# Kernel optimization log

Hardware: AMD Instinct MI355X
Metric: run time of the kernel (lower is better)

## Reference

```python
import jax, jax.numpy as jnp
import numpy as np

N_NODES = 50000
N_EDGES = 500000
NUM_RADIAL = 6
HIDDEN = 128

def swish(v):
    return v * jax.nn.sigmoid(v)

def setup_inputs() -> dict:
    key = jax.random.key(0)
    ks = jax.random.split(key, 8)
    x = jax.random.randint(ks[0], (N_NODES,), 0, 95, dtype=jnp.int32)
    rbf = jax.random.normal(ks[1], (N_EDGES, NUM_RADIAL), dtype=jnp.float32)
    i = jax.random.randint(ks[2], (N_EDGES,), 0, N_NODES, dtype=jnp.int32)
    j = jax.random.randint(ks[3], (N_EDGES,), 0, N_NODES, dtype=jnp.int32)
    sqrt3 = np.sqrt(3.0).astype(np.float32)
    emb_weight = jax.random.uniform(ks[4], (95, HIDDEN), minval=-sqrt3, maxval=sqrt3, dtype=jnp.float32)
    w_rbf0 = jax.random.normal(ks[5], (HIDDEN, NUM_RADIAL), dtype=jnp.float32) * 0.2
    b_rbf0 = jnp.zeros((HIDDEN,), dtype=jnp.float32)
    w_lin = jax.random.normal(ks[6], (HIDDEN, 3 * HIDDEN), dtype=jnpp.float32) if False else jax.random.normal(ks[6], (HIDDEN, 3 * HIDDEN), dtype=jnp.float32) * 0.05
    b_lin = jnp.zeros((HIDDEN,), dtype=jnp.float32)
    w_rbf1 = jax.random.normal(ks[7], (HIDDEN, NUM_RADIAL), dtype=jnp.float32) * 0.4
    return {"x": x, "rbf": rbf, "i": i, "j": j, "emb_weight": emb_weight,
            "w_rbf0": w_rbf0, "b_rbf0": b_rbf0, "w_lin": w_lin, "b_lin": b_lin,
            "w_rbf1": w_rbf1}

def reference(x, rbf, i, j, emb_weight, w_rbf0, b_rbf0, w_lin, b_lin, w_rbf1):
    # node embedding lookup: [N, H]
    h = emb_weight[x]
    # rbf0 = swish(rbf @ W0^T + b0): [E, H]
    rbf0 = swish(jnp.einsum('er,hr->eh', rbf, w_rbf0) + b_rbf0)
    # gather endpoint embeddings and concat with rbf0: [E, 3H]
    cat = jnp.concatenate([h[i], h[j], rbf0], axis=-1)
    e1 = swish(jnp.einsum('ek,hk->eh', cat, w_lin) + b_lin)
    e2 = jnp.einsum('er,hr->eh', rbf, w_rbf1) * e1
    return (e1, e2)
```

## Files before the change

### kernel.cpp

```cpp
#include <hip/hip_runtime.h>

#define HIDDEN 128
#define NRAD 6
#define NEMB 95

typedef short bf16x8 __attribute__((ext_vector_type(8)));
typedef float f32x4 __attribute__((ext_vector_type(4)));

__device__ __forceinline__ float fast_rcp(float x) { return __builtin_amdgcn_rcpf(x); }
__device__ __forceinline__ float swishf(float v) { return v * fast_rcp(1.0f + __expf(-v)); }
__device__ __forceinline__ short f2bf(float f) {
    union { float f; unsigned u; } c; c.f = f;
    unsigned r = (c.u + 0x7FFFu + ((c.u >> 16) & 1u)) >> 16;
    return (short)(unsigned short)r;
}
__device__ __forceinline__ float bf2f(unsigned short u) {
    union { unsigned u; float f; } c; c.u = ((unsigned)u) << 16; return c.f;
}
__device__ __forceinline__ unsigned pk(float lo, float hi) {
    return __builtin_amdgcn_perm(__float_as_uint(hi), __float_as_uint(lo), 0x07060302u);
}
__device__ __forceinline__ float xlo(unsigned u) {
    union { unsigned u; float f; } c; c.u = u << 16; return c.f;
}
__device__ __forceinline__ float xhi(unsigned u) {
    union { unsigned u; float f; } c; c.u = u & 0xffff0000u; return c.f;
}
__device__ __forceinline__ void barrier_lgkm() {
    asm volatile("s_waitcnt lgkmcnt(0)" ::: "memory");
    __builtin_amdgcn_s_barrier();
}
__device__ __forceinline__ void wait_lgkm() {
    asm volatile("s_waitcnt lgkmcnt(0)" ::: "memory");
}

__global__ void precompute_kernel(const float* __restrict__ emb,
                                  const float* __restrict__ w_lin,
                                  const float* __restrict__ b_lin,
                                  unsigned* __restrict__ pPair) {
    __shared__ __align__(16) float erow[HIDDEN];
    const int a = blockIdx.x;
    const int h = threadIdx.x;
    erow[h] = emb[a * HIDDEN + h];
    __syncthreads();
    float a1 = b_lin[h];
    float a2 = 0.f;
    const float* __restrict__ w1 = w_lin + h * 384;
    const float* __restrict__ w2 = w1 + HIDDEN;
#pragma unroll 8
    for (int k = 0; k < HIDDEN; ++k) {
        a1 += erow[k] * w1[k];
        a2 += erow[k] * w2[k];
    }
    const unsigned lo = (unsigned)(unsigned short)f2bf(a1);
    const unsigned hi = ((unsigned)(unsigned short)f2bf(a2)) << 16;
    pPair[a * HIDDEN + h] = hi | lo;
}

struct RawMD {
    float2 ra, rb, rc;
    int ii, jj;
};

__device__ __forceinline__ RawMD load_raw(int st, int l15, int n_edges,
                                          const int* __restrict__ iv,
                                          const int* __restrict__ jv,
                                          const float* __restrict__ rbf) {
    int e = st * 16 + l15;
    int ecl = (e < n_edges) ? e : (n_edges - 1);
    RawMD m;
    const float2* rp = reinterpret_cast<const float2*>(rbf + (size_t)ecl * NRAD);
    m.ra = rp[0];
    m.rb = rp[1];
    m.rc = rp[2];
    m.ii = iv[ecl];
    m.jj = jv[ecl];
    return m;
}

__global__ __launch_bounds__(256, 2)
void edge_mfma_kernel(const int* __restrict__ xv,
                      const float* __restrict__ rbf,
                      const int* __restrict__ iv,
                      const int* __restrict__ jv,
                      const float* __restrict__ w_rbf0,
                      const float* __restrict__ b_rbf0,
                      const float* __restrict__ w_rbf1,
                      const float* __restrict__ w_lin,
                      const unsigned* __restrict__ pPairG,
                      float* __restrict__ out_e1,
                      float* __restrict__ out_e2,
                      int n_edges, int tiles_per_block, int nt32, int n_rows) {
    __shared__ unsigned pps[NEMB * HIDDEN];
    __shared__ __align__(16) short fragS[2][16 * 132];
    __shared__ __align__(8) unsigned short stg[4][2][32 * 36];
    __shared__ __align__(16) short w1a[HIDDEN * 8];

    const int tid = threadIdx.x;

    {
        const int n = (n_rows < NEMB ? n_rows : NEMB) * HIDDEN;
        for (int s = tid; s < n; s += 256) pps[s] = pPairG[s];
    }
    if (tid < HIDDEN) {
        bf16x8 f1;
#pragma unroll
        for (int r = 0; r < NRAD; ++r) f1[r] = f2bf(w_rbf1[tid * NRAD + r]);
        f1[6] = 0; f1[7] = 0;
        *reinterpret_cast<bf16x8*>(&w1a[tid * 8]) = f1;
    }

    const int wid = tid >> 6;
    const int lane = tid & 63;
    const int l15 = lane & 15;
    const int lg = lane >> 4;

    const int kbase = wid * 32 + lg * 8;
    float w0r[8][6], b0r[8];
#pragma unroll
    for (int j = 0; j < 8; ++j) {
        const float2* wp = reinterpret_cast<const float2*>(w_rbf0 + (kbase + j) * NRAD);
        const float2 a = wp[0], b = wp[1], c = wp[2];
        w0r[j][0] = a.x; w0r[j][1] = a.y;
        w0r[j][2] = b.x; w0r[j][3] = b.y;
        w0r[j][4] = c.x; w0r[j][5] = c.y;
        b0r[j] = b_rbf0[kbase + j];
    }

    bf16x8 w3f[2][4];
#pragma unroll
    for (int n2 = 0; n2 < 2; ++n2) {
        const int h = (wid * 2 + n2) * 16 + l15;
        const float* wp = w_lin + h * 384 + 256;
#pragma unroll
        for (int ks = 0; ks < 4; ++ks) {
            const float4* s4 = reinterpret_cast<const float4*>(wp + (ks * 4 + lg) * 8);
            const float4 va = s4[0];
            const float4 vb = s4[1];
            bf16x8 fr;
            fr[0] = f2bf(va.x); fr[1] = f2bf(va.y);
            fr[2] = f2bf(va.z); fr[3] = f2bf(va.w);
            fr[4] = f2bf(vb.x); fr[5] = f2bf(vb.y);
            fr[6] = f2bf(vb.z); fr[7] = f2bf(vb.w);
            w3f[n2][ks] = fr;
        }
    }
    __syncthreads();

    const int bt = blockIdx.x * tiles_per_block;
    const int btEnd = min(bt + tiles_per_block, nt32);
    if (bt >= btEnd) return;

    const f32x4 zero4 = (f32x4){0.f, 0.f, 0.f, 0.f};

    RawMD c0 = load_raw(2 * bt,     l15, n_edges, iv, jv, rbf);
    RawMD c1 = load_raw(2 * bt + 1, l15, n_edges, iv, jv, rbf);
    RawMD x0 = load_raw(2 * bt + 2, l15, n_edges, iv, jv, rbf);
    RawMD x1 = load_raw(2 * bt + 3, l15, n_edges, iv, jv, rbf);
    int c0i = xv[c0.ii], c0j = xv[c0.jj];
    int c1i = xv[c1.ii], c1j = xv[c1.jj];

    for (int t = bt; t < btEnd; ++t) {
        RawMD p0 = load_raw(2 * (t + 2),     l15, n_edges, iv, jv, rbf);
        RawMD p1 = load_raw(2 * (t + 2) + 1, l15, n_edges, iv, jv, rbf);
        const int g0i = xv[x0.ii], g0j = xv[x0.jj];
        const int g1i = xv[x1.ii], g1j = xv[x1.jj];

        {
            float sv[8];
#pragma unroll
            for (int j = 0; j < 8; ++j) {
                float tv = b0r[j]
                         + c0.ra.x * w0r[j][0] + c0.ra.y * w0r[j][1]
                         + c0.rb.x * w0r[j][2] + c0.rb.y * w0r[j][3]
                         + c0.rc.x * w0r[j][4] + c0.rc.y * w0r[j][5];
                sv[j] = swishf(tv);
            }
            uint4 mf;
            mf.x = pk(sv[0], sv[1]); mf.y = pk(sv[2], sv[3]);
            mf.z = pk(sv[4], sv[5]); mf.w = pk(sv[6], sv[7]);
            *reinterpret_cast<uint4*>(&fragS[0][(wid * 4 + lg) * 132 + l15 * 8]) = mf;
        }
        {
            float sv[8];
#pragma unroll
            for (int j = 0; j < 8; ++j) {
                float tv = b0r[j]
                         + c1.ra.x * w0r[j][0] + c1.ra.y * w0r[j][1]
                         + c1.rb.x * w0r[j][2] + c1.rb.y * w0r[j][3]
                         + c1.rc.x * w0r[j][4] + c1.rc.y * w0r[j][5];
                sv[j] = swishf(tv);
            }
            uint4 mf;
            mf.x = pk(sv[0], sv[1]); mf.y = pk(sv[2], sv[3]);
            mf.z = pk(sv[4], sv[5]); mf.w = pk(sv[6], sv[7]);
            *reinterpret_cast<uint4*>(&fragS[1][(wid * 4 + lg) * 132 + l15 * 8]) = mf;
        }

        union { uint4 u; bf16x8 b; } rp0, rp1;
        rp0.u = (uint4){0u, 0u, 0u, 0u};
        rp1.u = (uint4){0u, 0u, 0u, 0u};
        if (lg == 0) {
            rp0.u.x = pk(c0.ra.x, c0.ra.y);
            rp0.u.y = pk(c0.rb.x, c0.rb.y);
            rp0.u.z = pk(c0.rc.x, c0.rc.y);
            rp1.u.x = pk(c1.ra.x, c1.ra.y);
            rp1.u.y = pk(c1.rb.x, c1.rb.y);
            rp1.u.z = pk(c1.rc.x, c1.rc.y);
        }
        f32x4 acc2[2][2];
#pragma unroll
        for (int n2 = 0; n2 < 2; ++n2) {
            const bf16x8 aw = *reinterpret_cast<const bf16x8*>(
                &w1a[((wid * 2 + n2) * 16 + l15) * 8]);
            acc2[0][n2] = __builtin_amdgcn_mfma_f32_16x16x32_bf16(aw, rp0.b, zero4, 0, 0, 0);
            acc2[1][n2] = __builtin_amdgcn_mfma_f32_16x16x32_bf16(aw, rp1.b, zero4, 0, 0, 0);
        }

        barrier_lgkm();

        f32x4 acc[2][2];
#pragma unroll
        for (int u = 0; u < 2; ++u) {
            bf16x8 bf[4];
#pragma unroll
            for (int ks = 0; ks < 4; ++ks)
                bf[ks] = *reinterpret_cast<const bf16x8*>(
                    &fragS[u][(ks * 4 + lg) * 132 + l15 * 8]);
#pragma unroll
            for (int n2 = 0; n2 < 2; ++n2) acc[u][n2] = zero4;
#pragma unroll
            for (int ks = 0; ks < 4; ++ks)
#pragma unroll
                for (int n2 = 0; n2 < 2; ++n2)
                    acc[u][n2] = __builtin_amdgcn_mfma_f32_16x16x32_bf16(
                        w3f[n2][ks], bf[ks], acc[u][n2], 0, 0, 0);
        }

        barrier_lgkm();

        if (t != bt) {
            const int tp = t - 1;
#pragma unroll
            for (int arr = 0; arr < 2; ++arr) {
                float* __restrict__ ob = arr ? out_e2 : out_e1;
#pragma unroll
                for (int s = 0; s < 4; ++s) {
                    const int e = 8 * s + (lane >> 3);
                    const uint2 u2v = *reinterpret_cast<const uint2*>(
                        &stg[wid][arr][e * 36 + (lane & 7) * 4]);
                    const int eg = tp * 32 + e;
                    if (eg < n_edges) {
                        f32x4 v;
                        v[0] = xlo(u2v.x); v[1] = xhi(u2v.x);
                        v[2] = xlo(u2v.y); v[3] = xhi(u2v.y);
                        *reinterpret_cast<f32x4*>(
                            ob + (size_t)eg * HIDDEN + wid * 32 + (lane & 7) * 4) = v;
                    }
                }
            }
        }
        wait_lgkm();

#pragma unroll
        for (int u = 0; u < 2; ++u) {
            const int xi = u ? c1i : c0i;
            const int xj = u ? c1j : c0j;
            const int row = u * 16 + l15;
#pragma unroll
            for (int n2 = 0; n2 < 2; ++n2) {
                const int ch0 = wid * 32 + n2 * 16 + lg * 4;
                const uint4 r1 = *reinterpret_cast<const uint4*>(&pps[xi * HIDDEN + ch0]);
                const uint4 r2 = *reinterpret_cast<const uint4*>(&pps[xj * HIDDEN + ch0]);
                float pv[4];
                pv[0] = bf2f((unsigned short)(r1.x & 0xffff)) + bf2f((unsigned short)(r2.x >> 16));
                pv[1] = bf2f((unsigned short)(r1.y & 0xffff)) + bf2f((unsigned short)(r2.y >> 16));
                pv[2] = bf2f((unsigned short)(r1.z & 0xffff)) + bf2f((unsigned short)(r2.z >> 16));
                pv[3] = bf2f((unsigned short)(r1.w & 0xffff)) + bf2f((unsigned short)(r2.w >> 16));
                float e1v[4], e2v[4];
#pragma unroll
                for (int q = 0; q < 4; ++q) {
                    const float s = acc[u][n2][q] + pv[q];
                    e1v[q] = swishf(s);
                    e2v[q] = acc2[u][n2][q] * e1v[q];
                }
                const int so = row * 36 + n2 * 16 + lg * 4;
                *reinterpret_cast<uint2*>(&stg[wid][0][so]) =
                    make_uint2(pk(e1v[0], e1v[1]), pk(e1v[2], e1v[3]));
                *reinterpret_cast<uint2*>(&stg[wid][1][so]) =
                    make_uint2(pk(e2v[0], e2v[1]), pk(e2v[2], e2v[3]));
            }
        }

        c0 = x0; c1 = x1; x0 = p0; x1 = p1;
        c0i = g0i; c0j = g0j; c1i = g1i; c1j = g1j;
    }

    wait_lgkm();
    {
        const int tp = btEnd - 1;
#pragma unroll
        for (int arr = 0; arr < 2; ++arr) {
            float* __restrict__ ob = arr ? out_e2 : out_e1;
#pragma unroll
            for (int s = 0; s < 4; ++s) {
                const int e = 8 * s + (lane >> 3);
                const uint2 u2v = *reinterpret_cast<const uint2*>(
                    &stg[wid][arr][e * 36 + (lane & 7) * 4]);
                const int eg = tp * 32 + e;
                if (eg < n_edges) {
                    f32x4 v;
                    v[0] = xlo(u2v.x); v[1] = xhi(u2v.x);
                    v[2] = xlo(u2v.y); v[3] = xhi(u2v.y);
                    *reinterpret_cast<f32x4*>(
                        ob + (size_t)eg * HIDDEN + wid * 32 + (lane & 7) * 4) = v;
                }
            }
        }
    }
}

extern "C" void kernel_launch(void* const* d_in, const int* in_sizes, int n_in,
                              void* d_out, int out_size, void* d_ws, size_t ws_size,
                              hipStream_t stream) {
    const int*   xv     = (const int*)  d_in[0];
    const float* rbf    = (const float*)d_in[1];
    const int*   iv     = (const int*)  d_in[2];
    const int*   jv     = (const int*)  d_in[3];
    const float* emb    = (const float*)d_in[4];
    const float* w_rbf0 = (const float*)d_in[5];
    const float* b_rbf0 = (const float*)d_in[6];
    const float* w_lin  = (const float*)d_in[7];
    const float* b_lin  = (const float*)d_in[8];
    const float* w_rbf1 = (const float*)d_in[9];

    const int n_edges = in_sizes[2];
    const int n_emb_rows = in_sizes[4] / HIDDEN;

    unsigned* pPair = (unsigned*)d_ws;

    float* out_e1 = (float*)d_out;
    float* out_e2 = out_e1 + (size_t)n_edges * HIDDEN;

    precompute_kernel<<<n_emb_rows, HIDDEN, 0, stream>>>(emb, w_lin, b_lin, pPair);

    const int nt32 = (n_edges + 31) / 32;
    const int grid = 512;
    const int tpb = (nt32 + grid - 1) / grid;
    edge_mfma_kernel<<<grid, 256, 0, stream>>>(xv, rbf, iv, jv,
                                               w_rbf0, b_rbf0, w_rbf1, w_lin,
                                               pPair, out_e1, out_e2,
                                               n_edges, tpb, nt32, n_emb_rows);
}
```

Measured before the change: 158.9 us.

## Split hidden channels across block pairs and compute rbf0 with MFMA

Each pair of blocks now covers one edge range, with each block handling half of the 128 hidden channels. This halves the per-block shared-memory table of precomputed embedding projections, and launch bounds rise to three blocks per CU on a 768-block grid. The rbf0 projection and its bias move from scalar FMAs to an MFMA, using a constant-1 input lane to fold in the bias, and each wave now handles 16 edges by 32 channels. The prefetch depth drops from two tiles to one. The trade-off is that every block reloads the edge metadata and recomputes the full rbf0 for its edges, so that work is duplicated across the pair.

```diff
diff --git a/kernel.cpp b/kernel.cpp
--- a/kernel.cpp
+++ b/kernel.cpp
@@ -3,6 +3,9 @@
 #define HIDDEN 128
 #define NRAD 6
 #define NEMB 95
+#define PRS 68
+#define FRS 132
+#define SRS 36
 
 typedef short bf16x8 __attribute__((ext_vector_type(8)));
 typedef float f32x4 __attribute__((ext_vector_type(4)));
@@ -78,7 +81,7 @@
     return m;
 }
 
-__global__ __launch_bounds__(256, 2)
+__global__ __launch_bounds__(256, 3)
 void edge_mfma_kernel(const int* __restrict__ xv,
                       const float* __restrict__ rbf,
                       const int* __restrict__ iv,
@@ -91,46 +94,35 @@
                       float* __restrict__ out_e1,
                       float* __restrict__ out_e2,
                       int n_edges, int tiles_per_block, int nt32, int n_rows) {
-    __shared__ unsigned pps[NEMB * HIDDEN];
-    __shared__ __align__(16) short fragS[2][16 * 132];
-    __shared__ __align__(8) unsigned short stg[4][2][32 * 36];
-    __shared__ __align__(16) short w1a[HIDDEN * 8];
+    __shared__ unsigned pps[NEMB * PRS];
+    __shared__ __align__(16) short fragS[2][16 * FRS];
+    __shared__ __align__(8) unsigned short stg[4][2][16 * SRS];
 
     const int tid = threadIdx.x;
+    const int chh = blockIdx.x & 1;
+    const int ebi = blockIdx.x >> 1;
 
     {
-        const int n = (n_rows < NEMB ? n_rows : NEMB) * HIDDEN;
-        for (int s = tid; s < n; s += 256) pps[s] = pPairG[s];
-    }
-    if (tid < HIDDEN) {
-        bf16x8 f1;
-#pragma unroll
-        for (int r = 0; r < NRAD; ++r) f1[r] = f2bf(w_rbf1[tid * NRAD + r]);
-        f1[6] = 0; f1[7] = 0;
-        *reinterpret_cast<bf16x8*>(&w1a[tid * 8]) = f1;
+        const int nr = (n_rows < NEMB ? n_rows : NEMB);
+        for (int s = tid; s < nr * 64; s += 256) {
+            const int a = s >> 6, c = s & 63;
+            pps[a * PRS + c] = pPairG[a * HIDDEN + chh * 64 + c];
+        }
     }
 
     const int wid = tid >> 6;
     const int lane = tid & 63;
     const int l15 = lane & 15;
     const int lg = lane >> 4;
-
-    const int kbase = wid * 32 + lg * 8;
-    float w0r[8][6], b0r[8];
-#pragma unroll
-    for (int j = 0; j < 8; ++j) {
-        const float2* wp = reinterpret_cast<const float2*>(w_rbf0 + (kbase + j) * NRAD);
-        const float2 a = wp[0], b = wp[1], c = wp[2];
-        w0r[j][0] = a.x; w0r[j][1] = a.y;
-        w0r[j][2] = b.x; w0r[j][3] = b.y;
-        w0r[j][4] = c.x; w0r[j][5] = c.y;
-        b0r[j] = b_rbf0[kbase + j];
-    }
+    const int u = wid >> 1;
+    const int c2 = wid & 1;
+    const int chbase = chh * 64 + c2 * 32;
 
     bf16x8 w3f[2][4];
+    bf16x8 w1f[2];
 #pragma unroll
     for (int n2 = 0; n2 < 2; ++n2) {
-        const int h = (wid * 2 + n2) * 16 + l15;
+        const int h = chbase + n2 * 16 + l15;
         const float* wp = w_lin + h * 384 + 256;
 #pragma unroll
         for (int ks = 0; ks < 4; ++ks) {
@@ -144,10 +136,29 @@
             fr[6] = f2bf(vb.z); fr[7] = f2bf(vb.w);
             w3f[n2][ks] = fr;
         }
+        bf16x8 f1;
+#pragma unroll
+        for (int r = 0; r < NRAD; ++r) f1[r] = f2bf(w_rbf1[h * NRAD + r]);
+        f1[6] = 0; f1[7] = 0;
+        w1f[n2] = f1;
+    }
+
+    bf16x8 aw0[2];
+#pragma unroll
+    for (int i = 0; i < 2; ++i) {
+        bf16x8 fr = (bf16x8){0, 0, 0, 0, 0, 0, 0, 0};
+        if (lg == 0) {
+            const int k = (2 * wid + i) * 16 + l15;
+#pragma unroll
+            for (int r = 0; r < NRAD; ++r) fr[r] = f2bf(w_rbf0[k * NRAD + r]);
+            fr[6] = f2bf(b_rbf0[k]);
+            fr[7] = 0;
+        }
+        aw0[i] = fr;
     }
     __syncthreads();
 
-    const int bt = blockIdx.x * tiles_per_block;
+    const int bt = ebi * tiles_per_block;
     const int btEnd = min(bt + tiles_per_block, nt32);
     if (bt >= btEnd) return;
 
@@ -155,86 +166,57 @@
 
     RawMD c0 = load_raw(2 * bt,     l15, n_edges, iv, jv, rbf);
     RawMD c1 = load_raw(2 * bt + 1, l15, n_edges, iv, jv, rbf);
-    RawMD x0 = load_raw(2 * bt + 2, l15, n_edges, iv, jv, rbf);
-    RawMD x1 = load_raw(2 * bt + 3, l15, n_edges, iv, jv, rbf);
-    int c0i = xv[c0.ii], c0j = xv[c0.jj];
-    int c1i = xv[c1.ii], c1j = xv[c1.jj];
 
     for (int t = bt; t < btEnd; ++t) {
-        RawMD p0 = load_raw(2 * (t + 2),     l15, n_edges, iv, jv, rbf);
-        RawMD p1 = load_raw(2 * (t + 2) + 1, l15, n_edges, iv, jv, rbf);
-        const int g0i = xv[x0.ii], g0j = xv[x0.jj];
-        const int g1i = xv[x1.ii], g1j = xv[x1.jj];
-
-        {
-            float sv[8];
-#pragma unroll
-            for (int j = 0; j < 8; ++j) {
-                float tv = b0r[j]
-                         + c0.ra.x * w0r[j][0] + c0.ra.y * w0r[j][1]
-                         + c0.rb.x * w0r[j][2] + c0.rb.y * w0r[j][3]
-                         + c0.rc.x * w0r[j][4] + c0.rc.y * w0r[j][5];
-                sv[j] = swishf(tv);
+        RawMD n0 = load_raw(2 * (t + 1),     l15, n_edges, iv, jv, rbf);
+        RawMD n1 = load_raw(2 * (t + 1) + 1, l15, n_edges, iv, jv, rbf);
+        const int exi = xv[u ? c1.ii : c0.ii];
+        const int exj = xv[u ? c1.jj : c0.jj];
+
+        union { uint4 q; bf16x8 b; } rp0, rp1;
+        rp0.q = (uint4){0u, 0u, 0u, 0u};
+        rp1.q = (uint4){0u, 0u, 0u, 0u};
+        if (lg == 0) {
+            rp0.q.x = pk(c0.ra.x, c0.ra.y);
+            rp0.q.y = pk(c0.rb.x, c0.rb.y);
+            rp0.q.z = pk(c0.rc.x, c0.rc.y);
+            rp0.q.w = pk(1.0f, 0.0f);
+            rp1.q.x = pk(c1.ra.x, c1.ra.y);
+            rp1.q.y = pk(c1.rb.x, c1.rb.y);
+            rp1.q.z = pk(c1.rc.x, c1.rc.y);
+            rp1.q.w = pk(1.0f, 0.0f);
+        }
+
+#pragma unroll
+        for (int s = 0; s < 2; ++s) {
+#pragma unroll
+            for (int i = 0; i < 2; ++i) {
+                const f32x4 cb = __builtin_amdgcn_mfma_f32_16x16x32_bf16(
+                    aw0[i], (s ? rp1.b : rp0.b), zero4, 0, 0, 0);
+                const uint2 wv = make_uint2(pk(swishf(cb[0]), swishf(cb[1])),
+                                            pk(swishf(cb[2]), swishf(cb[3])));
+                *reinterpret_cast<uint2*>(
+                    &fragS[s][l15 * FRS + (4 * (2 * wid + i) + lg) * 4]) = wv;
             }
-            uint4 mf;
-            mf.x = pk(sv[0], sv[1]); mf.y = pk(sv[2], sv[3]);
-            mf.z = pk(sv[4], sv[5]); mf.w = pk(sv[6], sv[7]);
-            *reinterpret_cast<uint4*>(&fragS[0][(wid * 4 + lg) * 132 + l15 * 8]) = mf;
-        }
-        {
-            float sv[8];
-#pragma unroll
-            for (int j = 0; j < 8; ++j) {
-                float tv = b0r[j]
-                         + c1.ra.x * w0r[j][0] + c1.ra.y * w0r[j][1]
-                         + c1.rb.x * w0r[j][2] + c1.rb.y * w0r[j][3]
-                         + c1.rc.x * w0r[j][4] + c1.rc.y * w0r[j][5];
-                sv[j] = swishf(tv);
-            }
-            uint4 mf;
-            mf.x = pk(sv[0], sv[1]); mf.y = pk(sv[2], sv[3]);
-            mf.z = pk(sv[4], sv[5]); mf.w = pk(sv[6], sv[7]);
-            *reinterpret_cast<uint4*>(&fragS[1][(wid * 4 + lg) * 132 + l15 * 8]) = mf;
-        }
-
-        union { uint4 u; bf16x8 b; } rp0, rp1;
-        rp0.u = (uint4){0u, 0u, 0u, 0u};
-        rp1.u = (uint4){0u, 0u, 0u, 0u};
-        if (lg == 0) {
-            rp0.u.x = pk(c0.ra.x, c0.ra.y);
-            rp0.u.y = pk(c0.rb.x, c0.rb.y);
-            rp0.u.z = pk(c0.rc.x, c0.rc.y);
-            rp1.u.x = pk(c1.ra.x, c1.ra.y);
-            rp1.u.y = pk(c1.rb.x, c1.rb.y);
-            rp1.u.z = pk(c1.rc.x, c1.rc.y);
-        }
-        f32x4 acc2[2][2];
-#pragma unroll
-        for (int n2 = 0; n2 < 2; ++n2) {
-            const bf16x8 aw = *reinterpret_cast<const bf16x8*>(
-                &w1a[((wid * 2 + n2) * 16 + l15) * 8]);
-            acc2[0][n2] = __builtin_amdgcn_mfma_f32_16x16x32_bf16(aw, rp0.b, zero4, 0, 0, 0);
-            acc2[1][n2] = __builtin_amdgcn_mfma_f32_16x16x32_bf16(aw, rp1.b, zero4, 0, 0, 0);
-        }
+        }
+
+        f32x4 acc2[2];
+#pragma unroll
+        for (int n2 = 0; n2 < 2; ++n2)
+            acc2[n2] = __builtin_amdgcn_mfma_f32_16x16x32_bf16(
+                w1f[n2], (u ? rp1.b : rp0.b), zero4, 0, 0, 0);
 
         barrier_lgkm();
 
-        f32x4 acc[2][2];
-#pragma unroll
-        for (int u = 0; u < 2; ++u) {
-            bf16x8 bf[4];
-#pragma unroll
-            for (int ks = 0; ks < 4; ++ks)
-                bf[ks] = *reinterpret_cast<const bf16x8*>(
-                    &fragS[u][(ks * 4 + lg) * 132 + l15 * 8]);
-#pragma unroll
-            for (int n2 = 0; n2 < 2; ++n2) acc[u][n2] = zero4;
-#pragma unroll
-            for (int ks = 0; ks < 4; ++ks)
-#pragma unroll
-                for (int n2 = 0; n2 < 2; ++n2)
-                    acc[u][n2] = __builtin_amdgcn_mfma_f32_16x16x32_bf16(
-                        w3f[n2][ks], bf[ks], acc[u][n2], 0, 0, 0);
+        f32x4 acc[2] = {zero4, zero4};
+#pragma unroll
+        for (int ks = 0; ks < 4; ++ks) {
+            const bf16x8 bf = *reinterpret_cast<const bf16x8*>(
+                &fragS[u][l15 * FRS + (8 * ks + 2 * lg) * 4]);
+#pragma unroll
+            for (int n2 = 0; n2 < 2; ++n2)
+                acc[n2] = __builtin_amdgcn_mfma_f32_16x16x32_bf16(
+                    w3f[n2][ks], bf, acc[n2], 0, 0, 0);
         }
 
         barrier_lgkm();
@@ -245,17 +227,17 @@
             for (int arr = 0; arr < 2; ++arr) {
                 float* __restrict__ ob = arr ? out_e2 : out_e1;
 #pragma unroll
-                for (int s = 0; s < 4; ++s) {
+                for (int s = 0; s < 2; ++s) {
                     const int e = 8 * s + (lane >> 3);
-                    const uint2 u2v = *reinterpret_cast<const uint2*>(
-                        &stg[wid][arr][e * 36 + (lane & 7) * 4]);
-                    const int eg = tp * 32 + e;
+                    const uint2 uv = *reinterpret_cast<const uint2*>(
+                        &stg[wid][arr][e * SRS + (lane & 7) * 4]);
+                    const int eg = tp * 32 + u * 16 + e;
                     if (eg < n_edges) {
                         f32x4 v;
-                        v[0] = xlo(u2v.x); v[1] = xhi(u2v.x);
-                        v[2] = xlo(u2v.y); v[3] = xhi(u2v.y);
+                        v[0] = xlo(uv.x); v[1] = xhi(uv.x);
+                        v[2] = xlo(uv.y); v[3] = xhi(uv.y);
                         *reinterpret_cast<f32x4*>(
-                            ob + (size_t)eg * HIDDEN + wid * 32 + (lane & 7) * 4) = v;
+                            ob + (size_t)eg * HIDDEN + chbase + (lane & 7) * 4) = v;
                     }
                 }
             }
@@ -263,37 +245,30 @@
         wait_lgkm();
 
 #pragma unroll
-        for (int u = 0; u < 2; ++u) {
-            const int xi = u ? c1i : c0i;
-            const int xj = u ? c1j : c0j;
-            const int row = u * 16 + l15;
-#pragma unroll
-            for (int n2 = 0; n2 < 2; ++n2) {
-                const int ch0 = wid * 32 + n2 * 16 + lg * 4;
-                const uint4 r1 = *reinterpret_cast<const uint4*>(&pps[xi * HIDDEN + ch0]);
-                const uint4 r2 = *reinterpret_cast<const uint4*>(&pps[xj * HIDDEN + ch0]);
-                float pv[4];
-                pv[0] = bf2f((unsigned short)(r1.x & 0xffff)) + bf2f((unsigned short)(r2.x >> 16));
-                pv[1] = bf2f((unsigned short)(r1.y & 0xffff)) + bf2f((unsigned short)(r2.y >> 16));
-                pv[2] = bf2f((unsigned short)(r1.z & 0xffff)) + bf2f((unsigned short)(r2.z >> 16));
-                pv[3] = bf2f((unsigned short)(r1.w & 0xffff)) + bf2f((unsigned short)(r2.w >> 16));
-                float e1v[4], e2v[4];
-#pragma unroll
-                for (int q = 0; q < 4; ++q) {
-                    const float s = acc[u][n2][q] + pv[q];
-                    e1v[q] = swishf(s);
-                    e2v[q] = acc2[u][n2][q] * e1v[q];
-                }
-                const int so = row * 36 + n2 * 16 + lg * 4;
-                *reinterpret_cast<uint2*>(&stg[wid][0][so]) =
-                    make_uint2(pk(e1v[0], e1v[1]), pk(e1v[2], e1v[3]));
-                *reinterpret_cast<uint2*>(&stg[wid][1][so]) =
-                    make_uint2(pk(e2v[0], e2v[1]), pk(e2v[2], e2v[3]));
+        for (int n2 = 0; n2 < 2; ++n2) {
+            const int ch0 = c2 * 32 + n2 * 16 + lg * 4;
+            const uint4 r1 = *reinterpret_cast<const uint4*>(&pps[exi * PRS + ch0]);
+            const uint4 r2 = *reinterpret_cast<const uint4*>(&pps[exj * PRS + ch0]);
+            float pv[4];
+            pv[0] = bf2f((unsigned short)(r1.x & 0xffff)) + bf2f((unsigned short)(r2.x >> 16));
+            pv[1] = bf2f((unsigned short)(r1.y & 0xffff)) + bf2f((unsigned short)(r2.y >> 16));
+            pv[2] = bf2f((unsigned short)(r1.z & 0xffff)) + bf2f((unsigned short)(r2.z >> 16));
+            pv[3] = bf2f((unsigned short)(r1.w & 0xffff)) + bf2f((unsigned short)(r2.w >> 16));
+            float e1v[4], e2v[4];
+#pragma unroll
+            for (int q = 0; q < 4; ++q) {
+                const float sm = acc[n2][q] + pv[q];
+                e1v[q] = swishf(sm);
+                e2v[q] = acc2[n2][q] * e1v[q];
             }
-        }
-
-        c0 = x0; c1 = x1; x0 = p0; x1 = p1;
-        c0i = g0i; c0j = g0j; c1i = g1i; c1j = g1j;
+            const int so = l15 * SRS + n2 * 16 + lg * 4;
+            *reinterpret_cast<uint2*>(&stg[wid][0][so]) =
+                make_uint2(pk(e1v[0], e1v[1]), pk(e1v[2], e1v[3]));
+            *reinterpret_cast<uint2*>(&stg[wid][1][so]) =
+                make_uint2(pk(e2v[0], e2v[1]), pk(e2v[2], e2v[3]));
+        }
+
+        c0 = n0; c1 = n1;
     }
 
     wait_lgkm();
@@ -303,17 +278,17 @@
         for (int arr = 0; arr < 2; ++arr) {
             float* __restrict__ ob = arr ? out_e2 : out_e1;
 #pragma unroll
-            for (int s = 0; s < 4; ++s) {
+            for (int s = 0; s < 2; ++s) {
                 const int e = 8 * s + (lane >> 3);
-                const uint2 u2v = *reinterpret_cast<const uint2*>(
-                    &stg[wid][arr][e * 36 + (lane & 7) * 4]);
-                const int eg = tp * 32 + e;
+                const uint2 uv = *reinterpret_cast<const uint2*>(
+                    &stg[wid][arr][e * SRS + (lane & 7) * 4]);
+                const int eg = tp * 32 + u * 16 + e;
                 if (eg < n_edges) {
                     f32x4 v;
-                    v[0] = xlo(u2v.x); v[1] = xhi(u2v.x);
-                    v[2] = xlo(u2v.y); v[3] = xhi(u2v.y);
+                    v[0] = xlo(uv.x); v[1] = xhi(uv.x);
+                    v[2] = xlo(uv.y); v[3] = xhi(uv.y);
                     *reinterpret_cast<f32x4*>(
-                        ob + (size_t)eg * HIDDEN + wid * 32 + (lane & 7) * 4) = v;
+                        ob + (size_t)eg * HIDDEN + chbase + (lane & 7) * 4) = v;
                 }
             }
         }
@@ -345,8 +320,9 @@
     precompute_kernel<<<n_emb_rows, HIDDEN, 0, stream>>>(emb, w_lin, b_lin, pPair);
 
     const int nt32 = (n_edges + 31) / 32;
-    const int grid = 512;
-    const int tpb = (nt32 + grid - 1) / grid;
+    const int grid = 768;
+    const int nEB = grid / 2;
+    const int tpb = (nt32 + nEB - 1) / nEB;
     edge_mfma_kernel<<<grid, 256, 0, stream>>>(xv, rbf, iv, jv,
                                                w_rbf0, b_rbf0, w_rbf1, w_lin,
                                                pPair, out_e1, out_e2,
```

New measurement: 176.2 us. 1.11x slower.
